# Kernel optimization log

Hardware: AMD Instinct MI355X
Metric: run time of the kernel (lower is better)

## Reference

```python
import jax, jax.numpy as jnp
import numpy as np

B, D, DEPTH, H, E, N, NC = 128, 192, 12, 3, 4, 65, 100
WIN_HALF = 3  # window_size=7 -> |i-j| <= 3


def _ln(x, g, b, eps=1e-5):
    m = x.mean(-1, keepdims=True)
    v = ((x - m) ** 2).mean(-1, keepdims=True)
    return (x - m) / jnp.sqrt(v + eps) * g + b


def _forward(x, conv_w, conv_b, pe_g, pe_b, cls_token, pos_embed,
             n1_g, n1_b, qkv_w, temp, proj_w, proj_b, n2_g, n2_b,
             gate_w, gate_b, e_w1, e_b1, e_w2, e_b2, attn_scale, mlp_scale,
             norm_g, norm_b, hc_w, hc_b, head_w, head_b):
    Bx = x.shape[0]
    # patch embed: conv with kernel==stride==4 is a blocked matmul
    p = x.reshape(Bx, 3, 8, 4, 8, 4).transpose(0, 2, 4, 1, 3, 5).reshape(Bx, 64, 48)
    t = p @ conv_w.reshape(D, 48).T + conv_b
    t = _ln(t, pe_g, pe_b)
    t = jnp.concatenate([jnp.broadcast_to(cls_token, (Bx, 1, D)), t], axis=1) + pos_embed
    Nn = t.shape[1]
    hd = D // H
    scale = hd ** -0.5
    idx = jnp.arange(Nn)
    # local-window attention mask (log of {0,1} -> {-inf,0})
    mask = jnp.where(jnp.abs(idx[:, None] - idx[None, :]) <= WIN_HALF, 0.0, -jnp.inf)
    for l in range(DEPTH):
        # --- attention ---
        y = _ln(t, n1_g[l], n1_b[l])
        qkv = (y @ qkv_w[l].T).reshape(Bx, Nn, 3, H, hd).transpose(2, 0, 3, 1, 4)
        q, k, v = qkv[0], qkv[1], qkv[2]
        a = (q @ k.transpose(0, 1, 3, 2)) * scale / temp[l]  # [B,H,N,N]
        a = jax.nn.softmax(a + mask, axis=-1)
        o = (a @ v).transpose(0, 2, 1, 3).reshape(Bx, Nn, D)
        o = o @ proj_w[l].T + proj_b[l]
        t = t + attn_scale[l] * o
        # --- top-2 MoE (dense-equivalent of the masked per-expert dispatch) ---
        y = _ln(t, n2_g[l], n2_b[l])
        g = jax.nn.softmax(y @ gate_w[l].T + gate_b[l], axis=-1)  # [B,N,E]
        tg, ti = jax.lax.top_k(g, 2)
        tg = tg / tg.sum(-1, keepdims=True)
        h = jax.nn.gelu(jnp.einsum('bnc,ehc->bneh', y, e_w1[l]) + e_b1[l], approximate=False)
        eo = jnp.einsum('bneh,ech->bnec', h, e_w2[l]) + e_b2[l]  # [B,N,E,C]
        sel = jnp.take_along_axis(eo, ti[..., None], axis=2)  # [B,N,2,C]
        mo = (sel * tg[..., None]).sum(axis=2)
        t = t + mlp_scale[l] * mo
    t = _ln(t, norm_g, norm_b)
    cls = t[:, 0]
    # hypercomplex linear head: out[:,k] += x[:,j] @ W[(k-j)%n].T
    xv = cls.reshape(Bx, E, D // E)
    perm = (jnp.arange(E)[:, None] - jnp.arange(E)[None, :]) % E  # [k,j] -> i
    hh = jnp.einsum('bjc,kjoc->bko', xv, hc_w[perm]).reshape(Bx, 2 * D) + hc_b
    hh = jax.nn.gelu(hh, approximate=False)
    return hh @ head_w.T + head_b


def setup_inputs() -> dict:
    ks = iter(jax.random.split(jax.random.key(0), 64))
    def rn(shape, s=0.02):
        return jax.random.normal(next(ks), shape, jnp.float32) * s
    return dict(
        x=jax.random.normal(next(ks), (B, 3, 32, 32), jnp.float32),
        conv_w=rn((D, 3, 4, 4)), conv_b=jnp.zeros((D,)),
        pe_g=jnp.ones((D,)), pe_b=jnp.zeros((D,)),
        cls_token=rn((1, 1, D)), pos_embed=rn((1, N, D)),
        n1_g=jnp.ones((DEPTH, D)), n1_b=jnp.zeros((DEPTH, D)),
        qkv_w=rn((DEPTH, 3 * D, D)), temp=jnp.ones((DEPTH, H, 1, 1)),
        proj_w=rn((DEPTH, D, D)), proj_b=jnp.zeros((DEPTH, D)),
        n2_g=jnp.ones((DEPTH, D)), n2_b=jnp.zeros((DEPTH, D)),
        gate_w=rn((DEPTH, E, D)), gate_b=jnp.zeros((DEPTH, E)),
        e_w1=rn((DEPTH, E, 2 * D, D)), e_b1=jnp.zeros((DEPTH, E, 2 * D)),
        e_w2=rn((DEPTH, E, D, 2 * D)), e_b2=jnp.zeros((DEPTH, E, D)),
        attn_scale=jnp.ones((DEPTH,)), mlp_scale=jnp.ones((DEPTH,)),
        norm_g=jnp.ones((D,)), norm_b=jnp.zeros((D,)),
        hc_w=rn((E, 2 * D // E, D // E)), hc_b=jnp.zeros((2 * D,)),
        head_w=rn((NC, 2 * D)), head_b=jnp.zeros((NC,)),
    )


def reference(x, conv_w, conv_b, pe_g, pe_b, cls_token, pos_embed,
              n1_g, n1_b, qkv_w, temp, proj_w, proj_b, n2_g, n2_b,
              gate_w, gate_b, e_w1, e_b1, e_w2, e_b2, attn_scale, mlp_scale,
              norm_g, norm_b, hc_w, hc_b, head_w, head_b):
    return _forward(x, conv_w, conv_b, pe_g, pe_b, cls_token, pos_embed,
                    n1_g, n1_b, qkv_w, temp, proj_w, proj_b, n2_g, n2_b,
                    gate_w, gate_b, e_w1, e_b1, e_w2, e_b2, attn_scale, mlp_scale,
                    norm_g, norm_b, hc_w, hc_b, head_w, head_b)
```

## Files before the change

### kernel.cpp

```cpp
#include <hip/hip_runtime.h>
#include <cmath>

#define ROWS 8320
#define DD   192

typedef __attribute__((ext_vector_type(8))) _Float16 half8;
typedef __attribute__((ext_vector_type(4))) float floatx4;

#define GLD16(gp, lp) __builtin_amdgcn_global_load_lds( \
    (const __attribute__((address_space(1))) void*)(gp), \
    (__attribute__((address_space(3))) void*)(lp), 16, 0, 0)

#define MFMA_F16 __builtin_amdgcn_mfma_f32_16x16x32_f16

__device__ __forceinline__ float gelu_f(float x) {
    return 0.5f * x * (1.0f + erff(x * 0.70710678118654752440f));
}

__device__ __forceinline__ float blk_sum_192(float v, float* sbuf) {
    int tid = threadIdx.x;
    sbuf[tid] = v;
    __syncthreads();
    for (int off = 96; off >= 3; off >>= 1) {
        if (tid < off) sbuf[tid] += sbuf[tid + off];
        __syncthreads();
    }
    float r = sbuf[0] + sbuf[1] + sbuf[2];
    __syncthreads();
    return r;
}

__device__ __forceinline__ void cvt8(const float* __restrict__ sp, _Float16* __restrict__ dp) {
    #pragma unroll
    for (int j = 0; j < 8; j++) dp[j] = (_Float16)sp[j];
}

__global__ __launch_bounds__(256) void cvt_all_kernel(
    const float* __restrict__ qkv_w, const float* __restrict__ proj_w,
    const float* __restrict__ e_w1, const float* __restrict__ e_w2,
    _Float16* __restrict__ qkvw_h, _Float16* __restrict__ projw_h,
    _Float16* __restrict__ ew1_h, _Float16* __restrict__ ew2_h)
{
    long i = (long)blockIdx.x * 256 + threadIdx.x;
    const long n_qkv  = (long)12 * 576 * 192 / 8;
    const long n_proj = (long)12 * 192 * 192 / 8;
    const long n_w1   = (long)12 * 1536 * 192 / 8;
    const long n_w2   = (long)12 * 192 * 192;
    if (i < n_qkv) { cvt8(qkv_w + i * 8, qkvw_h + i * 8); return; }
    i -= n_qkv;
    if (i < n_proj) { cvt8(proj_w + i * 8, projw_h + i * 8); return; }
    i -= n_proj;
    if (i < n_w1) { cvt8(e_w1 + i * 8, ew1_h + i * 8); return; }
    i -= n_w1;
    if (i < n_w2) {
        int l = (int)(i / (192 * 192));
        int rem = (int)(i % (192 * 192));
        int n = rem / 192, p = rem % 192;
        int c0 = p * 8;
        int e = c0 / 384, k0 = c0 % 384;
        cvt8(e_w2 + (((size_t)l * 4 + e) * 192 + n) * 384 + k0, ew2_h + i * 8);
    }
}

__global__ __launch_bounds__(192) void embed_kernel(
    const float* __restrict__ x, const float* __restrict__ conv_w,
    const float* __restrict__ conv_b, const float* __restrict__ pe_g,
    const float* __restrict__ pe_b, const float* __restrict__ cls_tok,
    const float* __restrict__ pos, float* __restrict__ t)
{
    __shared__ float patch[48];
    __shared__ float red[192];
    int blk = blockIdx.x;
    int b = blk / 65, n = blk % 65;
    int tid = threadIdx.x;
    if (n == 0) {
        t[(size_t)b * 65 * DD + tid] = cls_tok[tid] + pos[tid];
        return;
    }
    int p = n - 1, gy = p / 8, gx = p % 8;
    if (tid < 48) {
        int c = tid / 16, iy = (tid % 16) / 4, ix = tid % 4;
        patch[tid] = x[((size_t)b * 3 + c) * 1024 + (size_t)(gy * 4 + iy) * 32 + (gx * 4 + ix)];
    }
    __syncthreads();
    float s = conv_b[tid];
    const float* w = conv_w + (size_t)tid * 48;
    #pragma unroll
    for (int f = 0; f < 48; f++) s += patch[f] * w[f];
    float mean = blk_sum_192(s, red) * (1.0f / 192.0f);
    float d = s - mean;
    float var = blk_sum_192(d * d, red) * (1.0f / 192.0f);
    float o = d * rsqrtf(var + 1e-5f) * pe_g[tid] + pe_b[tid];
    t[((size_t)b * 65 + n) * DD + tid] = o + pos[(size_t)n * DD + tid];
}

__global__ __launch_bounds__(256) void ln_kernel(
    const float* __restrict__ in,
    float* __restrict__ yf, _Float16* __restrict__ yh,
    const float* __restrict__ g, const float* __restrict__ bb, long in_stride, int nrows,
    const float* __restrict__ gwm, const float* __restrict__ gb,
    int4* __restrict__ gwout)
{
    int wave = threadIdx.x >> 6, lane = threadIdx.x & 63;
    int r = blockIdx.x * 4 + wave;
    if (r >= nrows) return;
    const float* row = in + (size_t)r * in_stride;
    float v0 = row[lane], v1 = row[lane + 64], v2 = row[lane + 128];
    float s = v0 + v1 + v2;
    #pragma unroll
    for (int off = 32; off > 0; off >>= 1) s += __shfl_xor(s, off);
    float mean = s * (1.0f / 192.0f);
    float d0 = v0 - mean, d1 = v1 - mean, d2 = v2 - mean;
    float q = d0 * d0 + d1 * d1 + d2 * d2;
    #pragma unroll
    for (int off = 32; off > 0; off >>= 1) q += __shfl_xor(q, off);
    float rstd = rsqrtf(q * (1.0f / 192.0f) + 1e-5f);
    float o0 = d0 * rstd * g[lane] + bb[lane];
    float o1 = d1 * rstd * g[lane + 64] + bb[lane + 64];
    float o2 = d2 * rstd * g[lane + 128] + bb[lane + 128];
    if (yf) {
        float* yr = yf + (size_t)r * DD;
        yr[lane] = o0; yr[lane + 64] = o1; yr[lane + 128] = o2;
    }
    if (yh) {
        _Float16* yr = yh + (size_t)r * DD;
        yr[lane] = (_Float16)o0; yr[lane + 64] = (_Float16)o1; yr[lane + 128] = (_Float16)o2;
    }
    if (gwm) {
        float pe[4];
        #pragma unroll
        for (int e = 0; e < 4; e++) {
            const float* w = gwm + (size_t)e * DD;
            pe[e] = o0 * w[lane] + o1 * w[lane + 64] + o2 * w[lane + 128];
            #pragma unroll
            for (int off = 32; off > 0; off >>= 1) pe[e] += __shfl_xor(pe[e], off);
        }
        if (lane == 0) {
            #pragma unroll
            for (int e = 0; e < 4; e++) pe[e] += gb[e];
            float mx = fmaxf(fmaxf(pe[0], pe[1]), fmaxf(pe[2], pe[3]));
            float ex[4];
            #pragma unroll
            for (int e = 0; e < 4; e++) ex[e] = expf(pe[e] - mx);
            int i0 = 0;
            #pragma unroll
            for (int e = 1; e < 4; e++) if (ex[e] > ex[i0]) i0 = e;
            int i1 = (i0 == 0) ? 1 : 0;
            #pragma unroll
            for (int e = 0; e < 4; e++) if (e != i0 && ex[e] > ex[i1]) i1 = e;
            float denom = ex[i0] + ex[i1];
            int4 o4;
            o4.x = i0; o4.y = i1;
            o4.z = __float_as_int(ex[i0] / denom);
            o4.w = __float_as_int(ex[i1] / denom);
            gwout[r] = o4;
        }
    }
}

__global__ __launch_bounds__(256) void gate_build_kernel(
    const int4* __restrict__ gwrow, int* __restrict__ cnt,
    int* __restrict__ list, float* __restrict__ wlist, int rows)
{
    int r = blockIdx.x * 256 + threadIdx.x;
    int lane = threadIdx.x & 63;
    bool active = r < rows;
    int4 gv = active ? gwrow[r] : int4{-1, -1, 0, 0};
    #pragma unroll
    for (int e = 0; e < 4; e++) {
        bool sel = active && (gv.x == e || gv.y == e);
        int rank = (gv.x == e) ? 0 : 1;
        float w = (gv.x == e) ? __int_as_float(gv.z) : __int_as_float(gv.w);
        unsigned long long mask = __ballot(sel);
        int cw = __popcll(mask);
        if (cw) {
            int leader = __ffsll((long long)mask) - 1;
            int base = 0;
            if (lane == leader) base = atomicAdd(&cnt[e], cw);
            base = __shfl(base, leader);
            if (sel) {
                int idx = base + __popcll(mask & ((1ULL << lane) - 1ULL));
                list[(size_t)e * ROWS + idx] = (r << 1) | rank;
                wlist[(size_t)e * ROWS + idx] = w;
            }
        }
    }
}

template <int MODE>
__global__ __launch_bounds__(256) void gemm_h(
    const _Float16* __restrict__ A, const _Float16* __restrict__ W,
    int Nn, _Float16* __restrict__ outH, float* __restrict__ t,
    const float* __restrict__ bias, const float* __restrict__ scale)
{
    __shared__ __align__(16) _Float16 As[64 * 192];
    __shared__ __align__(16) _Float16 Ws[64 * 192];
    const int tid = threadIdx.x;
    const int lane = tid & 63, wave = tid >> 6;
    const int m0 = blockIdx.x * 64, n0 = blockIdx.y * 64;
    const int wm = (wave & 1) * 32, wn = (wave >> 1) * 32;
    const int lr = lane & 15, quad = lane >> 4;

    #pragma unroll
    for (int i = 0; i < 6; i++) {
        int s = (wave * 6 + i) * 64 + lane;
        int rr = s / 24, c = s % 24;
        GLD16(A + (size_t)(m0 + rr) * 192 + (c ^ (rr & 7)) * 8,
              (char*)As + (size_t)(wave * 6 + i) * 1024);
        GLD16(W + (size_t)(n0 + rr) * 192 + (c ^ (rr & 7)) * 8,
              (char*)Ws + (size_t)(wave * 6 + i) * 1024);
    }
    __syncthreads();

    floatx4 zero = {0.f, 0.f, 0.f, 0.f};
    floatx4 acc[2][2];
    acc[0][0] = zero; acc[0][1] = zero; acc[1][0] = zero; acc[1][1] = zero;

    #pragma unroll
    for (int m = 0; m < 6; m++) {
        int ch = m * 4 + quad;
        half8 a[2], w[2];
        #pragma unroll
        for (int ti = 0; ti < 2; ti++) {
            int ar = wm + ti * 16 + lr;
            a[ti] = *(const half8*)(As + ((size_t)ar * 24 + (ch ^ (ar & 7))) * 8);
            int cr = wn + ti * 16 + lr;
            w[ti] = *(const half8*)(Ws + ((size_t)cr * 24 + (ch ^ (cr & 7))) * 8);
        }
        #pragma unroll
        for (int ti = 0; ti < 2; ti++)
            #pragma unroll
            for (int tj = 0; tj < 2; tj++)
                acc[ti][tj] = MFMA_F16(a[ti], w[tj], acc[ti][tj], 0, 0, 0);
    }

    float sc = (MODE == 2) ? scale[0] : 0.f;
    #pragma unroll
    for (int ti = 0; ti < 2; ti++)
        #pragma unroll
        for (int tj = 0; tj < 2; tj++)
            #pragma unroll
            for (int r = 0; r < 4; r++) {
                int grow = m0 + wm + ti * 16 + quad * 4 + r;
                int gcol = n0 + wn + tj * 16 + lr;
                float v = acc[ti][tj][r];
                if (MODE == 0) {
                    float vp = __shfl_xor(v, 1);
                    if ((lane & 1) == 0) {
                        union { _Float16 h[2]; unsigned u; } pk;
                        pk.h[0] = (_Float16)v;
                        pk.h[1] = (_Float16)vp;
                        *(unsigned*)(outH + (size_t)grow * Nn + (gcol & ~1)) = pk.u;
                    }
                } else {
                    t[(size_t)grow * DD + gcol] += sc * (v + bias[gcol]);
                }
            }
}

__global__ __launch_bounds__(256) void moe_kernel(
    const _Float16* __restrict__ yh, const _Float16* __restrict__ w1,
    const _Float16* __restrict__ w2, const float* __restrict__ b1,
    const float* __restrict__ b2, const float* __restrict__ scale,
    const int* __restrict__ cnt, const int* __restrict__ list,
    const float* __restrict__ wlist, float* __restrict__ t)
{
    __shared__ __align__(16) _Float16 W1s[64 * 192];
    __shared__ __align__(16) _Float16 W2s[192 * 64];
    __shared__ __align__(16) _Float16 Hs[32 * 64];
    const int e  = blockIdx.y;
    const int cnte = cnt[e];
    const int r0 = blockIdx.x * 32;
    if (r0 >= cnte) return;
    const int tid = threadIdx.x;
    const int lane = tid & 63, wave = tid >> 6;
    const int lr = lane & 15, quad = lane >> 4;
    const int wr = (wave & 1) * 16;
    const int wc1 = (wave >> 1) * 16;
    const int wc2 = (wave >> 1) * 96;

    #pragma unroll
    for (int i = 0; i < 6; i++) {
        int s = (wave * 6 + i) * 64 + lane;
        int rr = s / 24, c = s % 24;
        GLD16(w1 + ((size_t)e * 384 + rr) * 192 + (c ^ (rr & 7)) * 8,
              (char*)W1s + (size_t)(wave * 6 + i) * 1024);
    }

    int sl = r0 + wr + lr;
    int rv = -1; float wv = 0.f;
    if (sl < cnte) {
        rv = list[(size_t)e * ROWS + sl];
        wv = wlist[(size_t)e * ROWS + sl];
    }
    int arow = (rv >= 0) ? (rv >> 1) : 0;

    half8 a[6];
    {
        const _Float16* ap = yh + (size_t)arow * 192 + quad * 8;
        #pragma unroll
        for (int m = 0; m < 6; m++) a[m] = *(const half8*)(ap + m * 32);
    }

    int rvr[4]; float bwr[4];
    #pragma unroll
    for (int r = 0; r < 4; r++) {
        rvr[r] = __shfl(rv, quad * 4 + r);
        bwr[r] = __shfl(wv, quad * 4 + r);
    }

    __syncthreads();

    floatx4 zero = {0.f, 0.f, 0.f, 0.f};
    floatx4 acc2[6];
    #pragma unroll
    for (int j = 0; j < 6; j++) acc2[j] = zero;

    for (int nc = 0; nc < 6; nc++) {
        int ncg = e * 6 + nc;
        #pragma unroll
        for (int i = 0; i < 6; i++) {
            int s = (wave * 6 + i) * 64 + lane;
            int n = s >> 3, c = s & 7;
            GLD16(w2 + (size_t)n * 1536 + (ncg * 8 + (c ^ (n & 7))) * 8,
                  (char*)W2s + (size_t)(wave * 6 + i) * 1024);
        }
        floatx4 acc1[2];
        acc1[0] = zero; acc1[1] = zero;
        #pragma unroll
        for (int m = 0; m < 6; m++) {
            int ch = m * 4 + quad;
            #pragma unroll
            for (int tc = 0; tc < 2; tc++) {
                int cr = wc1 + tc * 32 + lr;
                half8 w = *(const half8*)(W1s + ((size_t)cr * 24 + (ch ^ (cr & 7))) * 8);
                acc1[tc] = MFMA_F16(a[m], w, acc1[tc], 0, 0, 0);
            }
        }
        #pragma unroll
        for (int tc = 0; tc < 2; tc++)
            #pragma unroll
            for (int r = 0; r < 4; r++) {
                int hrow = wr + quad * 4 + r;
                int hcol = wc1 + tc * 32 + lr;
                float v = gelu_f(acc1[tc][r] + b1[64 * ncg + hcol]) * bwr[r];
                float vp = __shfl_xor(v, 1);
                if ((lane & 1) == 0) {
                    union { _Float16 h[2]; unsigned u; } pk;
                    pk.h[0] = (_Float16)v;
                    pk.h[1] = (_Float16)vp;
                    int cl = (hcol >> 3) ^ (hrow & 7);
                    *(unsigned*)(Hs + ((size_t)hrow * 8 + cl) * 8 + (hcol & 7)) = pk.u;
                }
            }
        __syncthreads();
        if (nc < 5) {
            #pragma unroll
            for (int i = 0; i < 6; i++) {
                int s = (wave * 6 + i) * 64 + lane;
                int rr = s / 24, c = s % 24;
                GLD16(w1 + ((size_t)e * 384 + (nc + 1) * 64 + rr) * 192 + (c ^ (rr & 7)) * 8,
                      (char*)W1s + (size_t)(wave * 6 + i) * 1024);
            }
        }
        #pragma unroll
        for (int kk = 0; kk < 2; kk++) {
            int ar = wr + lr;
            int ch = kk * 4 + quad;
            half8 ha = *(const half8*)(Hs + ((size_t)ar * 8 + (ch ^ (ar & 7))) * 8);
            #pragma unroll
            for (int tj = 0; tj < 6; tj++) {
                int cr = wc2 + tj * 16 + lr;
                half8 w = *(const half8*)(W2s + ((size_t)cr * 8 + (ch ^ (cr & 7))) * 8);
                acc2[tj] = MFMA_F16(ha, w, acc2[tj], 0, 0, 0);
            }
        }
        __syncthreads();
    }

    float sc = scale[0];
    #pragma unroll
    for (int tj = 0; tj < 6; tj++) {
        int gcol = wc2 + tj * 16 + lr;
        float b2v = b2[e * 192 + gcol];
        #pragma unroll
        for (int r = 0; r < 4; r++) {
            if (rvr[r] >= 0) {
                float v = sc * (acc2[tj][r] + bwr[r] * b2v);
                atomicAdd(&t[(size_t)(rvr[r] >> 1) * DD + gcol], v);
            }
        }
    }
}

__global__ __launch_bounds__(256) void attn_kernel(
    const _Float16* __restrict__ qkv, const float* __restrict__ temp,
    _Float16* __restrict__ o)
{
    __shared__ float q[65][66], k[65][66], v[65][66];
    __shared__ float p[65][9];
    int bh = blockIdx.x;
    int b = bh / 3, h = bh % 3;
    int tid = threadIdx.x;
    float coef = 0.125f / temp[h];
    const _Float16* base = qkv + (size_t)b * 65 * 576 + h * 64;
    for (int idx = tid; idx < 65 * 32; idx += 256) {
        int i = idx >> 5, d2 = (idx & 31) * 2;
        const _Float16* bp = base + (size_t)i * 576 + d2;
        q[i][d2] = (float)bp[0];   q[i][d2 + 1] = (float)bp[1];
        k[i][d2] = (float)bp[192]; k[i][d2 + 1] = (float)bp[193];
        v[i][d2] = (float)bp[384]; v[i][d2 + 1] = (float)bp[385];
    }
    __syncthreads();
    for (int idx = tid; idx < 65 * 7; idx += 256) {
        int i = idx / 7, jo = idx % 7;
        int j = i - 3 + jo;
        float s = -1e30f;
        if (j >= 0 && j < 65) {
            const float2* qr = (const float2*)&q[i][0];
            const float2* kr = (const float2*)&k[j][0];
            float acc = 0.f;
            #pragma unroll
            for (int d2 = 0; d2 < 32; d2++) {
                float2 aa = qr[d2], bb = kr[d2];
                acc += aa.x * bb.x + aa.y * bb.y;
            }
            s = acc * coef;
        }
        p[i][jo] = s;
    }
    __syncthreads();
    if (tid < 65) {
        float mx = -1e30f;
        #pragma unroll
        for (int jo = 0; jo < 7; jo++) mx = fmaxf(mx, p[tid][jo]);
        float ex[7], sum = 0.f;
        #pragma unroll
        for (int jo = 0; jo < 7; jo++) { ex[jo] = expf(p[tid][jo] - mx); sum += ex[jo]; }
        float inv = 1.0f / sum;
        #pragma unroll
        for (int jo = 0; jo < 7; jo++) p[tid][jo] = ex[jo] * inv;
    }
    __syncthreads();
    for (int idx = tid; idx < 65 * 32; idx += 256) {
        int i = idx >> 5, d2 = (idx & 31) * 2;
        float s0 = 0.f, s1 = 0.f;
        #pragma unroll
        for (int jo = 0; jo < 7; jo++) {
            int j = i - 3 + jo;
            if (j >= 0 && j < 65) {
                float pv = p[i][jo];
                s0 += pv * v[j][d2];
                s1 += pv * v[j][d2 + 1];
            }
        }
        union { _Float16 h2[2]; unsigned u; } pk;
        pk.h2[0] = (_Float16)s0; pk.h2[1] = (_Float16)s1;
        *(unsigned*)(o + ((size_t)b * 65 + i) * 192 + h * 64 + d2) = pk.u;
    }
}

__global__ __launch_bounds__(128) void head_kernel(
    const float* __restrict__ cls, const float* __restrict__ hc_w,
    const float* __restrict__ hc_b, const float* __restrict__ head_w,
    const float* __restrict__ head_b, float* __restrict__ out)
{
    __shared__ float c[192];
    __shared__ float hh[384];
    int b = blockIdx.x, tid = threadIdx.x;
    for (int i = tid; i < 192; i += 128) c[i] = cls[(size_t)b * 192 + i];
    __syncthreads();
    for (int i = tid; i < 384; i += 128) {
        int kx = i / 96, o = i % 96;
        float s = hc_b[i];
        #pragma unroll
        for (int j = 0; j < 4; j++) {
            int pp = (kx - j + 4) & 3;
            const float* w = hc_w + ((size_t)pp * 96 + o) * 48;
            const float* xv = c + j * 48;
            #pragma unroll
            for (int cc = 0; cc < 48; cc++) s += xv[cc] * w[cc];
        }
        hh[i] = gelu_f(s);
    }
    __syncthreads();
    for (int i = tid; i < 100; i += 128) {
        float s = head_b[i];
        const float* w = head_w + (size_t)i * 384;
        for (int kk = 0; kk < 384; kk++) s += hh[kk] * w[kk];
        out[(size_t)b * 100 + i] = s;
    }
}

extern "C" void kernel_launch(void* const* d_in, const int* in_sizes, int n_in,
                              void* d_out, int out_size, void* d_ws, size_t ws_size,
                              hipStream_t stream)
{
    const float* x        = (const float*)d_in[0];
    const float* conv_w   = (const float*)d_in[1];
    const float* conv_b   = (const float*)d_in[2];
    const float* pe_g     = (const float*)d_in[3];
    const float* pe_b     = (const float*)d_in[4];
    const float* cls_tok  = (const float*)d_in[5];
    const float* pos      = (const float*)d_in[6];
    const float* n1_g     = (const float*)d_in[7];
    const float* n1_b     = (const float*)d_in[8];
    const float* qkv_w    = (const float*)d_in[9];
    const float* temp     = (const float*)d_in[10];
    const float* proj_w   = (const float*)d_in[11];
    const float* proj_b   = (const float*)d_in[12];
    const float* n2_g     = (const float*)d_in[13];
    const float* n2_b     = (const float*)d_in[14];
    const float* gate_w   = (const float*)d_in[15];
    const float* gate_b   = (const float*)d_in[16];
    const float* e_w1     = (const float*)d_in[17];
    const float* e_b1     = (const float*)d_in[18];
    const float* e_w2     = (const float*)d_in[19];
    const float* e_b2     = (const float*)d_in[20];
    const float* attn_sc  = (const float*)d_in[21];
    const float* mlp_sc   = (const float*)d_in[22];
    const float* norm_g   = (const float*)d_in[23];
    const float* norm_b   = (const float*)d_in[24];
    const float* hc_w     = (const float*)d_in[25];
    const float* hc_b     = (const float*)d_in[26];
    const float* head_w   = (const float*)d_in[27];
    const float* head_b   = (const float*)d_in[28];

    char* base = (char*)d_ws;
    float*  t     = (float*)base;   base += (size_t)ROWS * DD * 4;
    int4*   gwrow = (int4*)base;    base += (size_t)ROWS * 16;
    int*    cnts  = (int*)base;     base += (size_t)12 * 4 * sizeof(int) + 64;
    int*    elist = (int*)base;     base += (size_t)4 * ROWS * 4;
    float*  ewls  = (float*)base;   base += (size_t)4 * ROWS * 4;
    float*  ycls  = (float*)base;   base += (size_t)128 * DD * 4;
    _Float16* yhb = (_Float16*)base; base += (size_t)ROWS * DD * 2;
    _Float16* qkvh = (_Float16*)base; base += (size_t)ROWS * 576 * 2;
    _Float16* osph = (_Float16*)base; base += (size_t)ROWS * DD * 2;
    _Float16* qkvw_h = (_Float16*)base; base += (size_t)12 * 576 * 192 * 2;
    _Float16* projw_h = (_Float16*)base; base += (size_t)12 * 192 * 192 * 2;
    _Float16* ew1_h = (_Float16*)base; base += (size_t)12 * 1536 * 192 * 2;
    _Float16* ew2_h = (_Float16*)base; base += (size_t)12 * 192 * 1536 * 2;

    hipMemsetAsync(cnts, 0, 12 * 4 * sizeof(int), stream);

    {
        long total = (long)12 * 576 * 192 / 8 + (long)12 * 192 * 192 / 8
                   + (long)12 * 1536 * 192 / 8 + (long)12 * 192 * 192;
        cvt_all_kernel<<<(int)((total + 255) / 256), 256, 0, stream>>>(
            qkv_w, proj_w, e_w1, e_w2, qkvw_h, projw_h, ew1_h, ew2_h);
    }

    embed_kernel<<<128 * 65, 192, 0, stream>>>(x, conv_w, conv_b, pe_g, pe_b, cls_tok, pos, t);

    for (int l = 0; l < 12; l++) {
        ln_kernel<<<ROWS / 4, 256, 0, stream>>>(
            t, nullptr, yhb, n1_g + l * DD, n1_b + l * DD, DD, ROWS,
            nullptr, nullptr, nullptr);
        gemm_h<0><<<dim3(130, 9), 256, 0, stream>>>(
            yhb, qkvw_h + (size_t)l * 576 * 192, 576, qkvh, nullptr, nullptr, nullptr);
        attn_kernel<<<128 * 3, 256, 0, stream>>>(qkvh, temp + l * 3, osph);
        gemm_h<2><<<dim3(130, 3), 256, 0, stream>>>(
            osph, projw_h + (size_t)l * 192 * 192, 192, nullptr, t,
            proj_b + l * DD, attn_sc + l);
        ln_kernel<<<ROWS / 4, 256, 0, stream>>>(
            t, nullptr, yhb, n2_g + l * DD, n2_b + l * DD, DD, ROWS,
            gate_w + (size_t)l * 4 * DD, gate_b + l * 4, gwrow);
        gate_build_kernel<<<(ROWS + 255) / 256, 256, 0, stream>>>(
            gwrow, cnts + l * 4, elist, ewls, ROWS);
        moe_kernel<<<dim3(260, 4), 256, 0, stream>>>(
            yhb, ew1_h + (size_t)l * 1536 * 192, ew2_h + (size_t)l * 192 * 1536,
            e_b1 + (size_t)l * 1536, e_b2 + (size_t)l * 4 * 192, mlp_sc + l,
            cnts + l * 4, elist, ewls, t);
    }

    ln_kernel<<<32, 256, 0, stream>>>(
        t, ycls, nullptr, norm_g, norm_b, (long)65 * DD, 128,
        nullptr, nullptr, nullptr);
    head_kernel<<<128, 128, 0, stream>>>(ycls, hc_w, hc_b, head_w, head_b, (float*)d_out);
}
```

Baseline: 1.099 ms.

## Read MoE expert weights straight from global memory and double-buffer Hs

The MoE kernel no longer stages W1 and W2 tiles in LDS through global_load_lds. Each wave now loads its MFMA weight fragments directly from global memory, relying on L2/L1 caching, and the Hs buffer is double-buffered so one barrier per chunk can be dropped. This cuts LDS footprint, which should raise occupancy, and removes staging syncs. The cost is many more scattered global loads per MFMA with less reuse across waves, leaving latency exposed.

```diff
diff --git a/kernel.cpp b/kernel.cpp
--- a/kernel.cpp
+++ b/kernel.cpp
@@ -265,9 +265,7 @@
     const int* __restrict__ cnt, const int* __restrict__ list,
     const float* __restrict__ wlist, float* __restrict__ t)
 {
-    __shared__ __align__(16) _Float16 W1s[64 * 192];
-    __shared__ __align__(16) _Float16 W2s[192 * 64];
-    __shared__ __align__(16) _Float16 Hs[32 * 64];
+    __shared__ __align__(16) _Float16 Hs[2][32 * 64];
     const int e  = blockIdx.y;
     const int cnte = cnt[e];
     const int r0 = blockIdx.x * 32;
@@ -279,14 +277,6 @@
     const int wc1 = (wave >> 1) * 16;
     const int wc2 = (wave >> 1) * 96;
 
-    #pragma unroll
-    for (int i = 0; i < 6; i++) {
-        int s = (wave * 6 + i) * 64 + lane;
-        int rr = s / 24, c = s % 24;
-        GLD16(w1 + ((size_t)e * 384 + rr) * 192 + (c ^ (rr & 7)) * 8,
-              (char*)W1s + (size_t)(wave * 6 + i) * 1024);
-    }
-
     int sl = r0 + wr + lr;
     int rv = -1; float wv = 0.f;
     if (sl < cnte) {
@@ -309,22 +299,16 @@
         bwr[r] = __shfl(wv, quad * 4 + r);
     }
 
-    __syncthreads();
+    const _Float16* w1e = w1 + (size_t)e * 384 * 192;
 
     floatx4 zero = {0.f, 0.f, 0.f, 0.f};
     floatx4 acc2[6];
     #pragma unroll
     for (int j = 0; j < 6; j++) acc2[j] = zero;
 
+    int cur = 0;
     for (int nc = 0; nc < 6; nc++) {
         int ncg = e * 6 + nc;
-        #pragma unroll
-        for (int i = 0; i < 6; i++) {
-            int s = (wave * 6 + i) * 64 + lane;
-            int n = s >> 3, c = s & 7;
-            GLD16(w2 + (size_t)n * 1536 + (ncg * 8 + (c ^ (n & 7))) * 8,
-                  (char*)W2s + (size_t)(wave * 6 + i) * 1024);
-        }
         floatx4 acc1[2];
         acc1[0] = zero; acc1[1] = zero;
         #pragma unroll
@@ -333,7 +317,7 @@
             #pragma unroll
             for (int tc = 0; tc < 2; tc++) {
                 int cr = wc1 + tc * 32 + lr;
-                half8 w = *(const half8*)(W1s + ((size_t)cr * 24 + (ch ^ (cr & 7))) * 8);
+                half8 w = *(const half8*)(w1e + (size_t)(nc * 64 + cr) * 192 + ch * 8);
                 acc1[tc] = MFMA_F16(a[m], w, acc1[tc], 0, 0, 0);
             }
         }
@@ -350,32 +334,23 @@
                     pk.h[0] = (_Float16)v;
                     pk.h[1] = (_Float16)vp;
                     int cl = (hcol >> 3) ^ (hrow & 7);
-                    *(unsigned*)(Hs + ((size_t)hrow * 8 + cl) * 8 + (hcol & 7)) = pk.u;
+                    *(unsigned*)(&Hs[cur][((size_t)hrow * 8 + cl) * 8 + (hcol & 7)]) = pk.u;
                 }
             }
         __syncthreads();
-        if (nc < 5) {
-            #pragma unroll
-            for (int i = 0; i < 6; i++) {
-                int s = (wave * 6 + i) * 64 + lane;
-                int rr = s / 24, c = s % 24;
-                GLD16(w1 + ((size_t)e * 384 + (nc + 1) * 64 + rr) * 192 + (c ^ (rr & 7)) * 8,
-                      (char*)W1s + (size_t)(wave * 6 + i) * 1024);
-            }
-        }
         #pragma unroll
         for (int kk = 0; kk < 2; kk++) {
             int ar = wr + lr;
             int ch = kk * 4 + quad;
-            half8 ha = *(const half8*)(Hs + ((size_t)ar * 8 + (ch ^ (ar & 7))) * 8);
+            half8 ha = *(const half8*)(&Hs[cur][((size_t)ar * 8 + (ch ^ (ar & 7))) * 8]);
             #pragma unroll
             for (int tj = 0; tj < 6; tj++) {
                 int cr = wc2 + tj * 16 + lr;
-                half8 w = *(const half8*)(W2s + ((size_t)cr * 8 + (ch ^ (cr & 7))) * 8);
+                half8 w = *(const half8*)(w2 + (size_t)cr * 1536 + ncg * 64 + ch * 8);
                 acc2[tj] = MFMA_F16(ha, w, acc2[tj], 0, 0, 0);
             }
         }
-        __syncthreads();
+        cur ^= 1;
     }
 
     float sc = scale[0];
```

Result: slower. 1.542 ms (+40.4%).
